# Performance work log

Measured on AMD Instinct MI355X. Metric: run time of the kernel, lower is better.

Reference implementation:

```python
import jax, jax.numpy as jnp
import numpy as np

# Fixed rotation angles (radians) standing in for IMAGE_ROTATE_DETECTOR_ANGLES[dataset]
ANGLES = [-0.5236, -0.2618, 0.0, 0.2618, 0.5236]
SHIFT_PIXELS = [1, 2, 3, 4, 5]  # shift_pixels_one_direction


def _shift_mats(H, W):
    # Direction enum iteration order: up, down, left, right; 'right' gets extra 0.
    mats = []
    for direction in ('up', 'down', 'left', 'right'):
        ps = SHIFT_PIXELS + ([0] if direction == 'right' else [])
        for p in ps:
            if direction == 'left':
                tx, ty = p, 0
            elif direction == 'right':
                tx, ty = -p, 0
            elif direction == 'up':
                tx, ty = 0, p
            else:  # down
                tx, ty = 0, -p
            mats.append([[1.0, 0.0, tx / float(W - 1)], [0.0, 1.0, ty / float(H - 1)]])
    return np.asarray(mats, dtype=np.float32)  # (S, 2, 3)


def _rotate_mats():
    mats = [[[np.cos(a), np.sin(a), 0.0], [-np.sin(a), np.cos(a), 0.0]] for a in ANGLES]
    return np.asarray(mats, dtype=np.float32)  # (R, 2, 3)


def _affine_grid(theta, H, W):
    # torch F.affine_grid with align_corners=True
    xs = jnp.linspace(-1.0, 1.0, W)
    ys = jnp.linspace(-1.0, 1.0, H)
    gx, gy = jnp.meshgrid(xs, ys)                       # (H, W)
    base = jnp.stack([gx, gy, jnp.ones_like(gx)], -1)   # (H, W, 3)
    return jnp.einsum('hwk,nik->nhwi', base, theta)     # (N, H, W, 2) -> (x, y)


def _grid_sample(img, grid):
    # torch F.grid_sample, bilinear, zero padding, align_corners=True
    N, C, H, W = img.shape
    ix = (grid[..., 0] + 1.0) * (W - 1) * 0.5           # (N, H, W)
    iy = (grid[..., 1] + 1.0) * (H - 1) * 0.5
    x0 = jnp.floor(ix)
    y0 = jnp.floor(iy)
    wx = ix - x0
    wy = iy - y0

    def corner(xi, yi, w):
        valid = (xi >= 0) & (xi <= W - 1) & (yi >= 0) & (yi <= H - 1)
        xc = jnp.clip(xi, 0, W - 1).astype(jnp.int32)
        yc = jnp.clip(yi, 0, H - 1).astype(jnp.int32)
        v = jax.vmap(lambda im, yy, xx: im[:, yy, xx])(img, yc, xc)  # (N, C, H, W)
        return v * (w * valid)[:, None]

    return (corner(x0, y0, (1 - wx) * (1 - wy))
            + corner(x0 + 1, y0, wx * (1 - wy))
            + corner(x0, y0 + 1, (1 - wx) * wy)
            + corner(x0 + 1, y0 + 1, wx * wy))


def setup_inputs() -> dict:
    key = jax.random.key(0)
    xs = jax.random.uniform(key, (4, 224, 224, 3), dtype=jnp.float32)
    return {"xs": xs}


def reference(xs):
    B, H, W, C = xs.shape
    x = jnp.transpose(xs, (0, 3, 1, 2))                 # (B, C, H, W)

    # Stage 1: pixel shifts. Output order = (shift s, image b) flattened as s*B + b.
    S_mats = jnp.asarray(_shift_mats(H, W))             # (S, 2, 3)
    S = S_mats.shape[0]
    x1 = jnp.broadcast_to(x[None], (S, B, C, H, W)).reshape(S * B, C, H, W)
    g1 = _affine_grid(jnp.repeat(S_mats, B, axis=0), H, W)
    x1 = _grid_sample(x1, g1)                           # (S*B, C, H, W)

    # Stage 2: rotations of the shifted batch. Order = (angle r, n) flattened as r*(S*B) + n.
    R_mats = jnp.asarray(_rotate_mats())                # (R, 2, 3)
    R = R_mats.shape[0]
    x2 = jnp.broadcast_to(x1[None], (R, S * B, C, H, W)).reshape(R * S * B, C, H, W)
    g2 = _affine_grid(jnp.repeat(R_mats, S * B, axis=0), H, W)
    out = _grid_sample(x2, g2)                          # (R*S*B, C, H, W)

    out = jnp.transpose(out, (0, 2, 3, 1))              # NHWC
    return out.reshape(R * S, B, H, W, C)
```

## Files before the change

### kernel.cpp

```cpp
#include <hip/hip_runtime.h>

namespace {

constexpr int H = 224, W = 224, B = 4, S = 21, R = 5;
constexpr int HW = H * W;

__constant__ float c_sin[5] = {-0.5000010604f, -0.2588196365f, 0.0f,
                                0.2588196365f,  0.5000010604f};
__constant__ float c_cos[5] = { 0.8660247916f,  0.9659256678f, 1.0f,
                                0.9659256678f,  0.8660247916f};

struct alignas(4) f3 { float x, y, z; };

__device__ __forceinline__ float vIn(int x) {
    return ((unsigned)x < (unsigned)W) ? 1.0f : 0.0f;
}
__device__ __forceinline__ int clampW(int x) {
    return min(max(x, 0), W - 1);
}
__device__ __forceinline__ void acc3(const f3& t, float wgt,
                                     float& a0, float& a1, float& a2) {
    a0 = fmaf(wgt, t.x, a0);
    a1 = fmaf(wgt, t.y, a1);
    a2 = fmaf(wgt, t.z, a2);
}

__global__ __launch_bounds__(256) void fused_shift_rotate(
    const float* __restrict__ xs, float* __restrict__ out) {
    int pix = blockIdx.x * 256 + threadIdx.x;
    int h = pix / W;
    int w = pix - h * W;
    int b = blockIdx.y;
    int rs = blockIdx.z;
    int r = rs / S;
    int s = rs - r * S;

    int tx = 0, ty = 0;
    if (s < 5)       ty = s + 1;
    else if (s < 10) ty = -(s - 4);
    else if (s < 15) tx = s - 9;
    else if (s < 20) tx = -(s - 14);

    float sr = c_sin[r], cr = c_cos[r];
    const float cx = 0.5f * (W - 1);
    float dx = (float)w - cx;
    float dy = (float)h - cx;
    float ix = fmaf(dy, sr, fmaf(dx, cr, cx));
    float iy = fmaf(dy, cr, fmaf(-dx, sr, cx));

    float x0f = floorf(ix), y0f = floorf(iy);
    int x0 = (int)x0f, y0 = (int)y0f;
    float wx = ix - x0f, wy = iy - y0f;
    float wxl = 1.0f - wx, wyl = 1.0f - wy;

    float vx0 = vIn(x0), vx1 = vIn(x0 + 1);
    float vy0 = vIn(y0), vy1 = vIn(y0 + 1);

    const f3* img = (const f3*)xs + (size_t)b * HW;

    float a0 = 0.f, a1 = 0.f, a2 = 0.f;

    if (tx & 1) {
        int xb = (2 * x0 + tx) >> 1;
        float cw0 = 0.5f * wxl * vx0 * vIn(xb);
        float cw1 = 0.5f * (wxl * vx0 + wx * vx1) * vIn(xb + 1);
        float cw2 = 0.5f * wx * vx1 * vIn(xb + 2);
        float rw0 = wyl * vy0;
        float rw1 = wy * vy1;
        int xc0 = clampW(xb), xc1 = clampW(xb + 1), xc2 = clampW(xb + 2);
        const f3* r0 = img + (size_t)clampW(y0) * W;
        const f3* r1 = img + (size_t)clampW(y0 + 1) * W;
        acc3(r0[xc0], rw0 * cw0, a0, a1, a2);
        acc3(r0[xc1], rw0 * cw1, a0, a1, a2);
        acc3(r0[xc2], rw0 * cw2, a0, a1, a2);
        acc3(r1[xc0], rw1 * cw0, a0, a1, a2);
        acc3(r1[xc1], rw1 * cw1, a0, a1, a2);
        acc3(r1[xc2], rw1 * cw2, a0, a1, a2);
    } else if (ty & 1) {
        int yb = (2 * y0 + ty) >> 1;
        float rw0 = 0.5f * wyl * vy0 * vIn(yb);
        float rw1 = 0.5f * (wyl * vy0 + wy * vy1) * vIn(yb + 1);
        float rw2 = 0.5f * wy * vy1 * vIn(yb + 2);
        float cw0 = wxl * vx0;
        float cw1 = wx * vx1;
        int xc0 = clampW(x0), xc1 = clampW(x0 + 1);
        const f3* r0 = img + (size_t)clampW(yb) * W;
        const f3* r1 = img + (size_t)clampW(yb + 1) * W;
        const f3* r2 = img + (size_t)clampW(yb + 2) * W;
        acc3(r0[xc0], rw0 * cw0, a0, a1, a2);
        acc3(r0[xc1], rw0 * cw1, a0, a1, a2);
        acc3(r1[xc0], rw1 * cw0, a0, a1, a2);
        acc3(r1[xc1], rw1 * cw1, a0, a1, a2);
        acc3(r2[xc0], rw2 * cw0, a0, a1, a2);
        acc3(r2[xc1], rw2 * cw1, a0, a1, a2);
    } else {
        int sx = tx >> 1, sy = ty >> 1;
        float ax0 = wxl * vx0 * vIn(x0 + sx);
        float ax1 = wx  * vx1 * vIn(x0 + 1 + sx);
        float ay0 = wyl * vy0 * vIn(y0 + sy);
        float ay1 = wy  * vy1 * vIn(y0 + 1 + sy);
        int xc0 = clampW(x0 + sx), xc1 = clampW(x0 + 1 + sx);
        const f3* r0 = img + (size_t)clampW(y0 + sy) * W;
        const f3* r1 = img + (size_t)clampW(y0 + 1 + sy) * W;
        acc3(r0[xc0], ay0 * ax0, a0, a1, a2);
        acc3(r0[xc1], ay0 * ax1, a0, a1, a2);
        acc3(r1[xc0], ay1 * ax0, a0, a1, a2);
        acc3(r1[xc1], ay1 * ax1, a0, a1, a2);
    }

    f3* op = (f3*)out + (size_t)(rs * B + b) * HW + pix;
    f3 v; v.x = a0; v.y = a1; v.z = a2;
    *op = v;
}

}

extern "C" void kernel_launch(void* const* d_in, const int* in_sizes, int n_in,
                              void* d_out, int out_size, void* d_ws, size_t ws_size,
                              hipStream_t stream) {
    const float* xs = (const float*)d_in[0];
    float* out = (float*)d_out;
    dim3 grid(HW / 256, B, R * S);
    fused_shift_rotate<<<grid, dim3(256), 0, stream>>>(xs, out);
}
```

Before: 282.4 us.

## Compute all 21 shifts per thread from a shared register neighborhood

Each thread now handles one rotation and one output pixel and produces all 21 shift variants. It loads an 8-wide horizontal and an 8-tall vertical neighborhood of source pixels into registers once and reuses them for every shift, so input gathers and rotation coordinate math are no longer repeated 21 times. The grid shrinks by a factor of 21, which raises register pressure and per-thread store work and lowers parallelism.

```diff
diff --git a/kernel.cpp b/kernel.cpp
--- a/kernel.cpp
+++ b/kernel.cpp
@@ -18,12 +18,6 @@
 __device__ __forceinline__ int clampW(int x) {
     return min(max(x, 0), W - 1);
 }
-__device__ __forceinline__ void acc3(const f3& t, float wgt,
-                                     float& a0, float& a1, float& a2) {
-    a0 = fmaf(wgt, t.x, a0);
-    a1 = fmaf(wgt, t.y, a1);
-    a2 = fmaf(wgt, t.z, a2);
-}
 
 __global__ __launch_bounds__(256) void fused_shift_rotate(
     const float* __restrict__ xs, float* __restrict__ out) {
@@ -31,15 +25,7 @@
     int h = pix / W;
     int w = pix - h * W;
     int b = blockIdx.y;
-    int rs = blockIdx.z;
-    int r = rs / S;
-    int s = rs - r * S;
-
-    int tx = 0, ty = 0;
-    if (s < 5)       ty = s + 1;
-    else if (s < 10) ty = -(s - 4);
-    else if (s < 15) tx = s - 9;
-    else if (s < 20) tx = -(s - 14);
+    int r = blockIdx.z;
 
     float sr = c_sin[r], cr = c_cos[r];
     const float cx = 0.5f * (W - 1);
@@ -55,62 +41,99 @@
 
     float vx0 = vIn(x0), vx1 = vIn(x0 + 1);
     float vy0 = vIn(y0), vy1 = vIn(y0 + 1);
+    float rwy0 = wyl * vy0, rwy1 = wy * vy1;
+    float cwx0 = wxl * vx0, cwx1 = wx * vx1;
 
-    const f3* img = (const f3*)xs + (size_t)b * HW;
+    const float* img = xs + (size_t)b * (HW * 3);
+    size_t obase = ((size_t)(r * S) * B + b) * (size_t)(HW * 3) + (size_t)pix * 3;
+    constexpr size_t splane = (size_t)B * HW * 3;
 
-    float a0 = 0.f, a1 = 0.f, a2 = 0.f;
-
-    if (tx & 1) {
-        int xb = (2 * x0 + tx) >> 1;
-        float cw0 = 0.5f * wxl * vx0 * vIn(xb);
-        float cw1 = 0.5f * (wxl * vx0 + wx * vx1) * vIn(xb + 1);
-        float cw2 = 0.5f * wx * vx1 * vIn(xb + 2);
-        float rw0 = wyl * vy0;
-        float rw1 = wy * vy1;
-        int xc0 = clampW(xb), xc1 = clampW(xb + 1), xc2 = clampW(xb + 2);
-        const f3* r0 = img + (size_t)clampW(y0) * W;
-        const f3* r1 = img + (size_t)clampW(y0 + 1) * W;
-        acc3(r0[xc0], rw0 * cw0, a0, a1, a2);
-        acc3(r0[xc1], rw0 * cw1, a0, a1, a2);
-        acc3(r0[xc2], rw0 * cw2, a0, a1, a2);
-        acc3(r1[xc0], rw1 * cw0, a0, a1, a2);
-        acc3(r1[xc1], rw1 * cw1, a0, a1, a2);
-        acc3(r1[xc2], rw1 * cw2, a0, a1, a2);
-    } else if (ty & 1) {
-        int yb = (2 * y0 + ty) >> 1;
-        float rw0 = 0.5f * wyl * vy0 * vIn(yb);
-        float rw1 = 0.5f * (wyl * vy0 + wy * vy1) * vIn(yb + 1);
-        float rw2 = 0.5f * wy * vy1 * vIn(yb + 2);
-        float cw0 = wxl * vx0;
-        float cw1 = wx * vx1;
-        int xc0 = clampW(x0), xc1 = clampW(x0 + 1);
-        const f3* r0 = img + (size_t)clampW(yb) * W;
-        const f3* r1 = img + (size_t)clampW(yb + 1) * W;
-        const f3* r2 = img + (size_t)clampW(yb + 2) * W;
-        acc3(r0[xc0], rw0 * cw0, a0, a1, a2);
-        acc3(r0[xc1], rw0 * cw1, a0, a1, a2);
-        acc3(r1[xc0], rw1 * cw0, a0, a1, a2);
-        acc3(r1[xc1], rw1 * cw1, a0, a1, a2);
-        acc3(r2[xc0], rw2 * cw0, a0, a1, a2);
-        acc3(r2[xc1], rw2 * cw1, a0, a1, a2);
-    } else {
-        int sx = tx >> 1, sy = ty >> 1;
-        float ax0 = wxl * vx0 * vIn(x0 + sx);
-        float ax1 = wx  * vx1 * vIn(x0 + 1 + sx);
-        float ay0 = wyl * vy0 * vIn(y0 + sy);
-        float ay1 = wy  * vy1 * vIn(y0 + 1 + sy);
-        int xc0 = clampW(x0 + sx), xc1 = clampW(x0 + 1 + sx);
-        const f3* r0 = img + (size_t)clampW(y0 + sy) * W;
-        const f3* r1 = img + (size_t)clampW(y0 + 1 + sy) * W;
-        acc3(r0[xc0], ay0 * ax0, a0, a1, a2);
-        acc3(r0[xc1], ay0 * ax1, a0, a1, a2);
-        acc3(r1[xc0], ay1 * ax0, a0, a1, a2);
-        acc3(r1[xc1], ay1 * ax1, a0, a1, a2);
+    {
+        float Hb[2][8][3];
+        const float* r0 = img + clampW(y0) * (W * 3);
+        const float* r1 = img + clampW(y0 + 1) * (W * 3);
+        #pragma unroll
+        for (int j = 0; j < 8; ++j) {
+            int xc = clampW(x0 - 3 + j) * 3;
+            const f3 t0 = *(const f3*)(r0 + xc);
+            const f3 t1 = *(const f3*)(r1 + xc);
+            Hb[0][j][0] = t0.x; Hb[0][j][1] = t0.y; Hb[0][j][2] = t0.z;
+            Hb[1][j][0] = t1.x; Hb[1][j][1] = t1.y; Hb[1][j][2] = t1.z;
+        }
+        constexpr int tx_tab[11] = {1, 2, 3, 4, 5, -1, -2, -3, -4, -5, 0};
+        #pragma unroll
+        for (int k = 0; k < 11; ++k) {
+            const int tx = tx_tab[k];
+            const int s = 10 + k;
+            float a[3];
+            if (tx & 1) {
+                const int j = ((tx - 1) >> 1) + 3;
+                int xb = x0 + ((tx - 1) >> 1);
+                float cw0 = 0.5f * wxl * vx0 * vIn(xb);
+                float cw1 = 0.5f * (wxl * vx0 + wx * vx1) * vIn(xb + 1);
+                float cw2 = 0.5f * wx * vx1 * vIn(xb + 2);
+                #pragma unroll
+                for (int c = 0; c < 3; ++c)
+                    a[c] = rwy0 * (cw0 * Hb[0][j][c] + cw1 * Hb[0][j + 1][c] + cw2 * Hb[0][j + 2][c])
+                         + rwy1 * (cw0 * Hb[1][j][c] + cw1 * Hb[1][j + 1][c] + cw2 * Hb[1][j + 2][c]);
+            } else {
+                const int sx = tx >> 1;
+                const int j = sx + 3;
+                float ax0 = cwx0 * vIn(x0 + sx);
+                float ax1 = cwx1 * vIn(x0 + 1 + sx);
+                #pragma unroll
+                for (int c = 0; c < 3; ++c)
+                    a[c] = rwy0 * (ax0 * Hb[0][j][c] + ax1 * Hb[0][j + 1][c])
+                         + rwy1 * (ax0 * Hb[1][j][c] + ax1 * Hb[1][j + 1][c]);
+            }
+            f3* op = (f3*)(out + obase + (size_t)s * splane);
+            f3 v; v.x = a[0]; v.y = a[1]; v.z = a[2];
+            *op = v;
+        }
     }
 
-    f3* op = (f3*)out + (size_t)(rs * B + b) * HW + pix;
-    f3 v; v.x = a0; v.y = a1; v.z = a2;
-    *op = v;
+    {
+        float Vb[8][2][3];
+        int xc0 = clampW(x0) * 3, xc1 = clampW(x0 + 1) * 3;
+        #pragma unroll
+        for (int i = 0; i < 8; ++i) {
+            const float* rr = img + clampW(y0 - 3 + i) * (W * 3);
+            const f3 t0 = *(const f3*)(rr + xc0);
+            const f3 t1 = *(const f3*)(rr + xc1);
+            Vb[i][0][0] = t0.x; Vb[i][0][1] = t0.y; Vb[i][0][2] = t0.z;
+            Vb[i][1][0] = t1.x; Vb[i][1][1] = t1.y; Vb[i][1][2] = t1.z;
+        }
+        constexpr int ty_tab[10] = {1, 2, 3, 4, 5, -1, -2, -3, -4, -5};
+        #pragma unroll
+        for (int k = 0; k < 10; ++k) {
+            const int ty = ty_tab[k];
+            const int s = k;
+            float a[3];
+            if (ty & 1) {
+                const int i = ((ty - 1) >> 1) + 3;
+                int yb = y0 + ((ty - 1) >> 1);
+                float rw0 = 0.5f * wyl * vy0 * vIn(yb);
+                float rw1 = 0.5f * (wyl * vy0 + wy * vy1) * vIn(yb + 1);
+                float rw2 = 0.5f * wy * vy1 * vIn(yb + 2);
+                #pragma unroll
+                for (int c = 0; c < 3; ++c)
+                    a[c] = cwx0 * (rw0 * Vb[i][0][c] + rw1 * Vb[i + 1][0][c] + rw2 * Vb[i + 2][0][c])
+                         + cwx1 * (rw0 * Vb[i][1][c] + rw1 * Vb[i + 1][1][c] + rw2 * Vb[i + 2][1][c]);
+            } else {
+                const int sy = ty >> 1;
+                const int i = sy + 3;
+                float ay0 = rwy0 * vIn(y0 + sy);
+                float ay1 = rwy1 * vIn(y0 + 1 + sy);
+                #pragma unroll
+                for (int c = 0; c < 3; ++c)
+                    a[c] = cwx0 * (ay0 * Vb[i][0][c] + ay1 * Vb[i + 1][0][c])
+                         + cwx1 * (ay0 * Vb[i][1][c] + ay1 * Vb[i + 1][1][c]);
+            }
+            f3* op = (f3*)(out + obase + (size_t)s * splane);
+            f3 v; v.x = a[0]; v.y = a[1]; v.z = a[2];
+            *op = v;
+        }
+    }
 }
 
 }
@@ -120,6 +143,6 @@
                               hipStream_t stream) {
     const float* xs = (const float*)d_in[0];
     float* out = (float*)d_out;
-    dim3 grid(HW / 256, B, R * S);
+    dim3 grid(HW / 256, B, R);
     fused_shift_rotate<<<grid, dim3(256), 0, stream>>>(xs, out);
 }
```

New measurement: 247.8 us. -12.3%, faster.
